# Optimization experiments

Hardware: AMD Instinct MI355X
Metric: run time of the kernel (lower is better)

Reference implementation:

```python
import jax, jax.numpy as jnp
import numpy as np

NUM_EMBEDDINGS = 1024
EMBEDDING_DIM = 256


def setup_inputs() -> dict:
    key = jax.random.key(0)
    k1, k2 = jax.random.split(key)
    input = jax.random.normal(k1, (64, 32, 32, EMBEDDING_DIM), dtype=jnp.float32)
    weight = jax.random.normal(k2, (NUM_EMBEDDINGS, EMBEDDING_DIM), dtype=jnp.float32)
    return {"input": input, "weight": weight}


def reference(input, weight):
    # Nearest-code lookup: argmin_k 0.5*||mu_k||^2 - <z, mu_k>  (scaled by 2 here,
    # matching torch: sqr - 2*cov). weight: [K, D], input: [..., D].
    sqr = jnp.sum(weight * weight, axis=1)                      # [K]
    cov = jnp.einsum('...j,kj->...k', input, weight)            # [..., K]
    indices = jnp.argmin(sqr - 2.0 * cov, axis=-1)              # [...]
    vectors = jnp.take(weight, indices, axis=0)                 # [..., D]
    # Straight-through estimator: values == vectors, grad flows to input.
    values = jax.lax.stop_gradient(vectors - input) + input
    return values, indices, vectors
```

## Files before the change

kernel.cpp:

```cpp
#include <hip/hip_runtime.h>


constexpr int N_TOK = 65536;
constexpr int KC    = 1024;
constexpr int D     = 256;

constexpr size_t IDX_OFF = (size_t)N_TOK * D;
constexpr size_t VEC_OFF = IDX_OFF + N_TOK;
constexpr int    OWL_CAP = 1 << 20;

#define MARGIN 12.0f

typedef __attribute__((ext_vector_type(8)))  short bf16x8;
typedef __attribute__((ext_vector_type(16))) float f32x16;

__device__ inline unsigned short f2bf(float x) {
    unsigned int u = __float_as_uint(x);
    unsigned int r = (u + 0x7FFFu + ((u >> 16) & 1u)) >> 16;
    return (unsigned short)r;
}

__device__ inline unsigned int fkey(float f) {
    unsigned int b = __float_as_uint(f);
    return (b & 0x80000000u) ? ~b : (b | 0x80000000u);
}

__global__ __launch_bounds__(64)
void vq_prep(const float* __restrict__ w, unsigned short* __restrict__ wbf,
             float* __restrict__ sqr, float* __restrict__ sqrp,
             int* __restrict__ cnt) {
    const int code = blockIdx.x;
    const int lane = threadIdx.x;
    float4 v = ((const float4*)w)[(size_t)code * 64 + lane];
    float s = v.x * v.x + v.y * v.y + v.z * v.z + v.w * v.w;
#pragma unroll
    for (int off = 32; off >= 1; off >>= 1) s += __shfl_xor(s, off, 64);
    unsigned short* d = wbf + (size_t)code * D + lane * 4;
    d[0] = f2bf(v.x); d[1] = f2bf(v.y); d[2] = f2bf(v.z); d[3] = f2bf(v.w);
    if (lane == 0) {
        sqr[code] = s;
        const int wi = code & 31;
        const int dest = (code >> 5) * 32 + ((wi >> 2) & 1) * 16
                       + (wi & 3) + 4 * (wi >> 3);
        sqrp[dest] = s;
    }
    if (code == 0 && lane == 0) *cnt = 0;
}

constexpr int CT   = 32;
constexpr int NSTG = KC / CT;
constexpr int LCAP = 5120;

struct __align__(16) P1Shared {
    unsigned short sbuf[3][CT * D];
    float sqr[KC];
    float sqrp[KC];
    int   list[LCAP];
    unsigned long long lcand[128];
    int   lcnt;
};

__device__ __forceinline__ void stage_issue(const char* __restrict__ srcbase,
                                            unsigned short* __restrict__ dstbuf,
                                            const int (&soff)[4], int tid) {
#pragma unroll
    for (int r = 0; r < 4; ++r) {
        __builtin_amdgcn_global_load_lds(
            (const __attribute__((address_space(1))) void*)(srcbase + soff[r]),
            (__attribute__((address_space(3))) void*)(dstbuf + (tid + r * 256) * 8),
            16, 0, 0);
    }
}

__global__ __launch_bounds__(256, 2)
void vq_scan(const float* __restrict__ input, const float* __restrict__ weight,
             const unsigned short* __restrict__ wbf, const float* __restrict__ sqr,
             const float* __restrict__ sqrp,
             int* __restrict__ cnt, int* __restrict__ owl,
             unsigned long long* __restrict__ cand) {
    __shared__ P1Shared sh;

    const int tid  = threadIdx.x;
    const int wave = tid >> 6;
    const int lane = tid & 63;
    const int cl   = lane & 31;
    const int hi   = lane >> 5;
    const int row_base_blk = blockIdx.x * 128;
    const char* wbfB = (const char*)wbf;

    if (tid == 0) sh.lcnt = 0;
    if (tid < 128) sh.lcand[tid] = 0xFFFFFFFFFFFFFFFFULL;
    ((float4*)sh.sqr)[tid]  = ((const float4*)sqr)[tid];
    ((float4*)sh.sqrp)[tid] = ((const float4*)sqrp)[tid];

    int soff[4];
#pragma unroll
    for (int r = 0; r < 4; ++r) {
        const int sl = tid + r * 256;
        soff[r] = (sl & 31) * 512 + (sl >> 5) * 16;
    }

    bf16x8 afr[16];
    {
        const float* ar = input + (size_t)(row_base_blk + wave * 32 + cl) * D;
#pragma unroll
        for (int kt = 0; kt < 16; ++kt) {
            const int k0 = kt * 16 + hi * 8;
            float4 f0 = *(const float4*)(ar + k0);
            float4 f1 = *(const float4*)(ar + k0 + 4);
            bf16x8 v;
            v[0] = (short)f2bf(f0.x); v[1] = (short)f2bf(f0.y);
            v[2] = (short)f2bf(f0.z); v[3] = (short)f2bf(f0.w);
            v[4] = (short)f2bf(f1.x); v[5] = (short)f2bf(f1.y);
            v[6] = (short)f2bf(f1.z); v[7] = (short)f2bf(f1.w);
            afr[kt] = v;
        }
    }

    float rmin = 3.4e38f;

    __syncthreads();

    stage_issue(wbfB, sh.sbuf[0], soff, tid);
    stage_issue(wbfB + 16384, sh.sbuf[1], soff, tid);

    for (int s = 0; s < NSTG; ++s) {
        if (s == NSTG - 1) asm volatile("s_waitcnt vmcnt(0)" ::: "memory");
        else               asm volatile("s_waitcnt vmcnt(4)" ::: "memory");
        __builtin_amdgcn_sched_barrier(0);
        __builtin_amdgcn_s_barrier();
        __builtin_amdgcn_sched_barrier(0);
        if (s + 2 < NSTG)
            stage_issue(wbfB + (s + 2) * 16384, sh.sbuf[(s + 2) % 3], soff, tid);

        const unsigned short* sb = sh.sbuf[s % 3] + (size_t)lane * 8;
        f32x16 acc = {0.f,0.f,0.f,0.f, 0.f,0.f,0.f,0.f,
                      0.f,0.f,0.f,0.f, 0.f,0.f,0.f,0.f};
#pragma unroll
        for (int h = 0; h < 2; ++h) {
            bf16x8 b[8];
#pragma unroll
            for (int kk = 0; kk < 8; ++kk)
                b[kk] = *(const bf16x8*)(sb + (h * 8 + kk) * 512);
#pragma unroll
            for (int kk = 0; kk < 8; ++kk)
                acc = __builtin_amdgcn_mfma_f32_32x32x16_bf16(b[kk], afr[h * 8 + kk], acc, 0, 0, 0);
        }

        const int c0 = s * CT;
        const float4* sp = (const float4*)(sh.sqrp + c0 + hi * 16);
        float4 q0 = sp[0], q1 = sp[1], q2 = sp[2], q3 = sp[3];
        float sc[16];
        sc[0]=q0.x-2.0f*acc[0];  sc[1]=q0.y-2.0f*acc[1];
        sc[2]=q0.z-2.0f*acc[2];  sc[3]=q0.w-2.0f*acc[3];
        sc[4]=q1.x-2.0f*acc[4];  sc[5]=q1.y-2.0f*acc[5];
        sc[6]=q1.z-2.0f*acc[6];  sc[7]=q1.w-2.0f*acc[7];
        sc[8]=q2.x-2.0f*acc[8];  sc[9]=q2.y-2.0f*acc[9];
        sc[10]=q2.z-2.0f*acc[10]; sc[11]=q2.w-2.0f*acc[11];
        sc[12]=q3.x-2.0f*acc[12]; sc[13]=q3.y-2.0f*acc[13];
        sc[14]=q3.z-2.0f*acc[14]; sc[15]=q3.w-2.0f*acc[15];

        float m = fminf(fminf(fminf(sc[0], sc[1]), fminf(sc[2], sc[3])),
                        fminf(fminf(sc[4], sc[5]), fminf(sc[6], sc[7])));
        m = fminf(m, fminf(fminf(fminf(sc[8], sc[9]), fminf(sc[10], sc[11])),
                           fminf(fminf(sc[12], sc[13]), fminf(sc[14], sc[15]))));
        m = fminf(m, __shfl_xor(m, 32, 64));
        rmin = fminf(rmin, m);
        const float thr = rmin + MARGIN;

        const int lrow = wave * 32 + cl;
#pragma unroll
        for (int r = 0; r < 16; ++r) {
            const bool flag = (sc[r] <= thr);
            unsigned long long mask = __ballot(flag);
            if (mask) {
                const int leader = __builtin_ctzll(mask);
                const int nact   = __popcll(mask);
                const int prefix = __popcll(mask & ((1ULL << lane) - 1ULL));
                int wbase = 0;
                if (lane == leader) wbase = atomicAdd(&sh.lcnt, nact);
                wbase = __shfl(wbase, leader, 64);
                if (flag) {
                    const int code = c0 + (r & 3) + 8 * (r >> 2) + 4 * hi;
                    const int pos  = wbase + prefix;
                    if (pos < LCAP) {
                        sh.list[pos] = (lrow << 10) | code;
                    } else {
                        int g = atomicAdd(cnt, 1);
                        if (g < OWL_CAP)
                            owl[g] = ((row_base_blk + lrow) << 10) | code;
                    }
                }
            }
        }
    }

    __syncthreads();

    {
        const int n  = min(sh.lcnt, LCAP);
        const int sw = tid >> 4;
        const int sl = tid & 15;
        const float4* in4 = (const float4*)input;
        const float4* w4  = (const float4*)weight;
        for (int e = sw; e < n; e += 16) {
            const int ent  = sh.list[e];
            const int lrow = ent >> 10;
            const int code = ent & 1023;
            const float4* zr = in4 + (size_t)(row_base_blk + lrow) * 64;
            const float4* wr = w4 + (size_t)code * 64;
            float s = 0.f;
#pragma unroll
            for (int j = 0; j < 4; ++j) {
                float4 za = zr[sl + 16 * j];
                float4 wa = wr[sl + 16 * j];
                s = fmaf(za.x, wa.x, s);
                s = fmaf(za.y, wa.y, s);
                s = fmaf(za.z, wa.z, s);
                s = fmaf(za.w, wa.w, s);
            }
#pragma unroll
            for (int off = 1; off <= 8; off <<= 1) s += __shfl_xor(s, off, 16);
            if (sl == 0) {
                const float score = sh.sqr[code] - 2.0f * s;
                unsigned long long key =
                    ((unsigned long long)fkey(score) << 32) | (unsigned int)code;
                atomicMin(&sh.lcand[lrow], key);
            }
        }
    }
    __syncthreads();

    if (tid < 128) cand[row_base_blk + tid] = sh.lcand[tid];
}

__global__ __launch_bounds__(256)
void vq_cleanup(const float* __restrict__ input, const float* __restrict__ weight,
                const float* __restrict__ sqr, const int* __restrict__ owl,
                const int* __restrict__ cnt, unsigned long long* __restrict__ cand) {
    const int m = min(*cnt, OWL_CAP);
    if (m == 0) return;
    __shared__ float zrow[D];
    __shared__ unsigned long long best;
    const int tid = threadIdx.x;
    for (int e = blockIdx.x; e < m; e += gridDim.x) {
        const int grow = owl[e] >> 10;
        if (tid == 0) best = 0xFFFFFFFFFFFFFFFFULL;
        if (tid < 64) ((float4*)zrow)[tid] = ((const float4*)input)[(size_t)grow * 64 + tid];
        __syncthreads();
        for (int cc = 0; cc < 4; ++cc) {
            const int code = tid * 4 + cc;
            const float4* wr = (const float4*)weight + (size_t)code * 64;
            float s = 0.f;
            for (int k = 0; k < 64; ++k) {
                float4 wa = wr[k];
                s = fmaf(zrow[4 * k],     wa.x, s);
                s = fmaf(zrow[4 * k + 1], wa.y, s);
                s = fmaf(zrow[4 * k + 2], wa.z, s);
                s = fmaf(zrow[4 * k + 3], wa.w, s);
            }
            const float score = sqr[code] - 2.0f * s;
            unsigned long long key =
                ((unsigned long long)fkey(score) << 32) | (unsigned int)code;
            atomicMin(&best, key);
        }
        __syncthreads();
        if (tid == 0) cand[grow] = best;
        __syncthreads();
    }
}

__global__ __launch_bounds__(256)
void vq_finish(const float* __restrict__ weight,
               const unsigned long long* __restrict__ cand,
               float* __restrict__ out) {
    __shared__ int fin[64];
    const int tid  = threadIdx.x;
    const int row0 = blockIdx.x * 64;
    if (tid < 64) {
        int idx = (int)(cand[row0 + tid] & 1023ULL);
        fin[tid] = idx;
        out[IDX_OFF + row0 + tid] = (float)idx;
    }
    __syncthreads();
    const float4* w4 = (const float4*)weight;
    float4* out4 = (float4*)out;
#pragma unroll
    for (int k = 0; k < 16; ++k) {
        int i = tid + k * 256;
        int r = i >> 6, q = i & 63;
        float4 v = w4[(size_t)fin[r] * 64 + q];
        size_t o = (size_t)(row0 + r) * 64 + q;
        out4[o] = v;
        out4[VEC_OFF / 4 + o] = v;
    }
}

extern "C" void kernel_launch(void* const* d_in, const int* in_sizes, int n_in,
                              void* d_out, int out_size, void* d_ws, size_t ws_size,
                              hipStream_t stream) {
    const float* input  = (const float*)d_in[0];
    const float* weight = (const float*)d_in[1];
    float* out = (float*)d_out;

    unsigned short* wbf = (unsigned short*)d_ws;
    float* sqr  = (float*)((char*)d_ws + 524288);
    float* sqrp = (float*)((char*)d_ws + 528384);
    int*   cnt  = (int*)((char*)d_ws + 532480);
    unsigned long long* cand = (unsigned long long*)((char*)d_ws + 536576);

    int* owl = (int*)out;

    vq_prep   <<<KC, 64, 0, stream>>>(weight, wbf, sqr, sqrp, cnt);
    vq_scan   <<<N_TOK / 128, 256, 0, stream>>>(input, weight, wbf, sqr, sqrp, cnt, owl, cand);
    vq_cleanup<<<256, 256, 0, stream>>>(input, weight, sqr, owl, cnt, cand);
    vq_finish <<<N_TOK / 64, 256, 0, stream>>>(weight, cand, out);
}
```

Before: 305.1 us.

## Widen scan blocks to 512 threads with per-wave candidate lists and score prefilter

The scan kernel now runs 512-thread blocks covering 256 rows, with 64-code stages that are double-buffered instead of triple-buffered. Each codebook tile loaded into LDS is therefore reused by twice as many rows. Candidate collection no longer uses a shared atomic counter. Each wave builds its own segment through a wave prefix scan and stores a truncated score key, and the fp32 rescoring pass skips entries whose key exceeds that row's final threshold. The cost is one block per CU, a synchronous barrier with only one stage of prefetch, and more shuffle work per tile.

```diff
diff --git a/kernel.cpp b/kernel.cpp
--- a/kernel.cpp
+++ b/kernel.cpp
@@ -40,24 +40,26 @@
     if (lane == 0) {
         sqr[code] = s;
         const int wi = code & 31;
-        const int dest = (code >> 5) * 32 + ((wi >> 2) & 1) * 16
+        const int dest = (code & ~31) + ((wi >> 2) & 1) * 16
                        + (wi & 3) + 4 * (wi >> 3);
         sqrp[dest] = s;
     }
     if (code == 0 && lane == 0) *cnt = 0;
 }
 
-constexpr int CT   = 32;
+constexpr int CT   = 64;
 constexpr int NSTG = KC / CT;
-constexpr int LCAP = 5120;
+constexpr int WCAP = 1280;
+constexpr int ROWS = 256;
 
 struct __align__(16) P1Shared {
-    unsigned short sbuf[3][CT * D];
+    unsigned short sbuf[2][CT * D];
     float sqr[KC];
     float sqrp[KC];
-    int   list[LCAP];
-    unsigned long long lcand[128];
-    int   lcnt;
+    int   list[8 * WCAP];
+    unsigned long long lcand[ROWS];
+    unsigned short tk[ROWS];
+    int   lcnt[8];
 };
 
 __device__ __forceinline__ void stage_issue(const char* __restrict__ srcbase,
@@ -67,12 +69,12 @@
     for (int r = 0; r < 4; ++r) {
         __builtin_amdgcn_global_load_lds(
             (const __attribute__((address_space(1))) void*)(srcbase + soff[r]),
-            (__attribute__((address_space(3))) void*)(dstbuf + (tid + r * 256) * 8),
+            (__attribute__((address_space(3))) void*)(dstbuf + (tid + r * 512) * 8),
             16, 0, 0);
     }
 }
 
-__global__ __launch_bounds__(256, 2)
+__global__ __launch_bounds__(512, 1)
 void vq_scan(const float* __restrict__ input, const float* __restrict__ weight,
              const unsigned short* __restrict__ wbf, const float* __restrict__ sqr,
              const float* __restrict__ sqrp,
@@ -85,19 +87,21 @@
     const int lane = tid & 63;
     const int cl   = lane & 31;
     const int hi   = lane >> 5;
-    const int row_base_blk = blockIdx.x * 128;
+    const int row_base_blk = blockIdx.x * ROWS;
     const char* wbfB = (const char*)wbf;
 
-    if (tid == 0) sh.lcnt = 0;
-    if (tid < 128) sh.lcand[tid] = 0xFFFFFFFFFFFFFFFFULL;
-    ((float4*)sh.sqr)[tid]  = ((const float4*)sqr)[tid];
-    ((float4*)sh.sqrp)[tid] = ((const float4*)sqrp)[tid];
+    if (tid < 8) sh.lcnt[tid] = 0;
+    if (tid < 256) {
+        sh.lcand[tid] = 0xFFFFFFFFFFFFFFFFULL;
+        ((float4*)sh.sqr)[tid]  = ((const float4*)sqr)[tid];
+        ((float4*)sh.sqrp)[tid] = ((const float4*)sqrp)[tid];
+    }
 
     int soff[4];
 #pragma unroll
     for (int r = 0; r < 4; ++r) {
-        const int sl = tid + r * 256;
-        soff[r] = (sl & 31) * 512 + (sl >> 5) * 16;
+        const int sl = tid + r * 512;
+        soff[r] = (sl & 63) * 512 + (sl >> 6) * 16;
     }
 
     bf16x8 afr[16];
@@ -118,120 +122,139 @@
     }
 
     float rmin = 3.4e38f;
+    int   wcur = 0;
 
     __syncthreads();
 
     stage_issue(wbfB, sh.sbuf[0], soff, tid);
-    stage_issue(wbfB + 16384, sh.sbuf[1], soff, tid);
 
     for (int s = 0; s < NSTG; ++s) {
-        if (s == NSTG - 1) asm volatile("s_waitcnt vmcnt(0)" ::: "memory");
-        else               asm volatile("s_waitcnt vmcnt(4)" ::: "memory");
-        __builtin_amdgcn_sched_barrier(0);
-        __builtin_amdgcn_s_barrier();
-        __builtin_amdgcn_sched_barrier(0);
-        if (s + 2 < NSTG)
-            stage_issue(wbfB + (s + 2) * 16384, sh.sbuf[(s + 2) % 3], soff, tid);
-
-        const unsigned short* sb = sh.sbuf[s % 3] + (size_t)lane * 8;
-        f32x16 acc = {0.f,0.f,0.f,0.f, 0.f,0.f,0.f,0.f,
-                      0.f,0.f,0.f,0.f, 0.f,0.f,0.f,0.f};
-#pragma unroll
-        for (int h = 0; h < 2; ++h) {
-            bf16x8 b[8];
-#pragma unroll
-            for (int kk = 0; kk < 8; ++kk)
-                b[kk] = *(const bf16x8*)(sb + (h * 8 + kk) * 512);
-#pragma unroll
-            for (int kk = 0; kk < 8; ++kk)
-                acc = __builtin_amdgcn_mfma_f32_32x32x16_bf16(b[kk], afr[h * 8 + kk], acc, 0, 0, 0);
-        }
-
+        __syncthreads();
+        if (s + 1 < NSTG)
+            stage_issue(wbfB + (s + 1) * 32768, sh.sbuf[(s + 1) & 1], soff, tid);
+
+        const unsigned short* sbb = sh.sbuf[s & 1];
         const int c0 = s * CT;
-        const float4* sp = (const float4*)(sh.sqrp + c0 + hi * 16);
-        float4 q0 = sp[0], q1 = sp[1], q2 = sp[2], q3 = sp[3];
-        float sc[16];
-        sc[0]=q0.x-2.0f*acc[0];  sc[1]=q0.y-2.0f*acc[1];
-        sc[2]=q0.z-2.0f*acc[2];  sc[3]=q0.w-2.0f*acc[3];
-        sc[4]=q1.x-2.0f*acc[4];  sc[5]=q1.y-2.0f*acc[5];
-        sc[6]=q1.z-2.0f*acc[6];  sc[7]=q1.w-2.0f*acc[7];
-        sc[8]=q2.x-2.0f*acc[8];  sc[9]=q2.y-2.0f*acc[9];
-        sc[10]=q2.z-2.0f*acc[10]; sc[11]=q2.w-2.0f*acc[11];
-        sc[12]=q3.x-2.0f*acc[12]; sc[13]=q3.y-2.0f*acc[13];
-        sc[14]=q3.z-2.0f*acc[14]; sc[15]=q3.w-2.0f*acc[15];
-
-        float m = fminf(fminf(fminf(sc[0], sc[1]), fminf(sc[2], sc[3])),
-                        fminf(fminf(sc[4], sc[5]), fminf(sc[6], sc[7])));
-        m = fminf(m, fminf(fminf(fminf(sc[8], sc[9]), fminf(sc[10], sc[11])),
-                           fminf(fminf(sc[12], sc[13]), fminf(sc[14], sc[15]))));
-        m = fminf(m, __shfl_xor(m, 32, 64));
-        rmin = fminf(rmin, m);
-        const float thr = rmin + MARGIN;
-
-        const int lrow = wave * 32 + cl;
-#pragma unroll
-        for (int r = 0; r < 16; ++r) {
-            const bool flag = (sc[r] <= thr);
-            unsigned long long mask = __ballot(flag);
-            if (mask) {
-                const int leader = __builtin_ctzll(mask);
-                const int nact   = __popcll(mask);
-                const int prefix = __popcll(mask & ((1ULL << lane) - 1ULL));
-                int wbase = 0;
-                if (lane == leader) wbase = atomicAdd(&sh.lcnt, nact);
-                wbase = __shfl(wbase, leader, 64);
-                if (flag) {
-                    const int code = c0 + (r & 3) + 8 * (r >> 2) + 4 * hi;
-                    const int pos  = wbase + prefix;
-                    if (pos < LCAP) {
-                        sh.list[pos] = (lrow << 10) | code;
-                    } else {
-                        int g = atomicAdd(cnt, 1);
-                        if (g < OWL_CAP)
-                            owl[g] = ((row_base_blk + lrow) << 10) | code;
+
+#pragma unroll
+        for (int t = 0; t < 2; ++t) {
+            const unsigned short* sb = sbb + (size_t)(hi * 64 + t * 32 + cl) * 8;
+            f32x16 acc = {0.f,0.f,0.f,0.f, 0.f,0.f,0.f,0.f,
+                          0.f,0.f,0.f,0.f, 0.f,0.f,0.f,0.f};
+#pragma unroll
+            for (int h = 0; h < 2; ++h) {
+                bf16x8 b[8];
+#pragma unroll
+                for (int kk = 0; kk < 8; ++kk)
+                    b[kk] = *(const bf16x8*)(sb + (size_t)(h * 8 + kk) * 1024);
+#pragma unroll
+                for (int kk = 0; kk < 8; ++kk)
+                    acc = __builtin_amdgcn_mfma_f32_32x32x16_bf16(b[kk], afr[h * 8 + kk], acc, 0, 0, 0);
+            }
+
+            const float4* sp = (const float4*)(sh.sqrp + c0 + t * 32 + hi * 16);
+            float4 q0 = sp[0], q1 = sp[1], q2 = sp[2], q3 = sp[3];
+            float sc[16];
+            sc[0]=q0.x-2.0f*acc[0];   sc[1]=q0.y-2.0f*acc[1];
+            sc[2]=q0.z-2.0f*acc[2];   sc[3]=q0.w-2.0f*acc[3];
+            sc[4]=q1.x-2.0f*acc[4];   sc[5]=q1.y-2.0f*acc[5];
+            sc[6]=q1.z-2.0f*acc[6];   sc[7]=q1.w-2.0f*acc[7];
+            sc[8]=q2.x-2.0f*acc[8];   sc[9]=q2.y-2.0f*acc[9];
+            sc[10]=q2.z-2.0f*acc[10]; sc[11]=q2.w-2.0f*acc[11];
+            sc[12]=q3.x-2.0f*acc[12]; sc[13]=q3.y-2.0f*acc[13];
+            sc[14]=q3.z-2.0f*acc[14]; sc[15]=q3.w-2.0f*acc[15];
+
+            float m = fminf(fminf(fminf(sc[0], sc[1]), fminf(sc[2], sc[3])),
+                            fminf(fminf(sc[4], sc[5]), fminf(sc[6], sc[7])));
+            m = fminf(m, fminf(fminf(fminf(sc[8], sc[9]), fminf(sc[10], sc[11])),
+                               fminf(fminf(sc[12], sc[13]), fminf(sc[14], sc[15]))));
+            m = fminf(m, __shfl_xor(m, 32, 64));
+            rmin = fminf(rmin, m);
+            const float thr = rmin + MARGIN;
+
+            unsigned m16 = 0u;
+#pragma unroll
+            for (int r = 0; r < 16; ++r)
+                m16 |= (sc[r] <= thr) ? (1u << r) : 0u;
+            const int cntl = __popc(m16);
+            int incl = cntl;
+#pragma unroll
+            for (int off = 1; off < 64; off <<= 1) {
+                int v = __shfl_up(incl, off, 64);
+                if (lane >= off) incl += v;
+            }
+            const int total = __shfl(incl, 63, 64);
+            if (total) {
+                const int base = wcur + (incl - cntl);
+                int* seg = sh.list + wave * WCAP;
+#pragma unroll
+                for (int r = 0; r < 16; ++r) {
+                    if (m16 & (1u << r)) {
+                        const int pos  = base + __popc(m16 & ((1u << r) - 1u));
+                        const int code = c0 + t * 32 + (r & 3) + 8 * (r >> 2) + 4 * hi;
+                        if (pos < WCAP) {
+                            const unsigned skey = fkey(sc[r]) >> 16;
+                            seg[pos] = (int)((skey << 16) | ((unsigned)cl << 10)
+                                             | (unsigned)code);
+                        } else {
+                            int g = atomicAdd(cnt, 1);
+                            if (g < OWL_CAP)
+                                owl[g] = ((row_base_blk + wave * 32 + cl) << 10) | code;
+                        }
                     }
                 }
+                wcur += total;
             }
         }
     }
 
+    if (hi == 0) {
+        unsigned t32 = (fkey(rmin + MARGIN) >> 16) + 1u;
+        sh.tk[wave * 32 + cl] = (unsigned short)(t32 > 0xFFFFu ? 0xFFFFu : t32);
+    }
+    if (lane == 0) sh.lcnt[wave] = (wcur < WCAP) ? wcur : WCAP;
+
     __syncthreads();
 
     {
-        const int n  = min(sh.lcnt, LCAP);
         const int sw = tid >> 4;
         const int sl = tid & 15;
         const float4* in4 = (const float4*)input;
         const float4* w4  = (const float4*)weight;
-        for (int e = sw; e < n; e += 16) {
-            const int ent  = sh.list[e];
-            const int lrow = ent >> 10;
-            const int code = ent & 1023;
-            const float4* zr = in4 + (size_t)(row_base_blk + lrow) * 64;
-            const float4* wr = w4 + (size_t)code * 64;
-            float s = 0.f;
-#pragma unroll
-            for (int j = 0; j < 4; ++j) {
-                float4 za = zr[sl + 16 * j];
-                float4 wa = wr[sl + 16 * j];
-                s = fmaf(za.x, wa.x, s);
-                s = fmaf(za.y, wa.y, s);
-                s = fmaf(za.z, wa.z, s);
-                s = fmaf(za.w, wa.w, s);
-            }
-#pragma unroll
-            for (int off = 1; off <= 8; off <<= 1) s += __shfl_xor(s, off, 16);
-            if (sl == 0) {
-                const float score = sh.sqr[code] - 2.0f * s;
-                unsigned long long key =
-                    ((unsigned long long)fkey(score) << 32) | (unsigned int)code;
-                atomicMin(&sh.lcand[lrow], key);
+        for (int seg = 0; seg < 8; ++seg) {
+            const int n = sh.lcnt[seg];
+            const int* lp = sh.list + seg * WCAP;
+            for (int e = sw; e < n; e += 32) {
+                const unsigned ent = (unsigned)lp[e];
+                const int lrow = seg * 32 + (int)((ent >> 10) & 31u);
+                if ((ent >> 16) > (unsigned)sh.tk[lrow]) continue;
+                const int code = (int)(ent & 1023u);
+                const float4* zr = in4 + (size_t)(row_base_blk + lrow) * 64;
+                const float4* wr = w4 + (size_t)code * 64;
+                float s = 0.f;
+#pragma unroll
+                for (int j = 0; j < 4; ++j) {
+                    float4 za = zr[sl + 16 * j];
+                    float4 wa = wr[sl + 16 * j];
+                    s = fmaf(za.x, wa.x, s);
+                    s = fmaf(za.y, wa.y, s);
+                    s = fmaf(za.z, wa.z, s);
+                    s = fmaf(za.w, wa.w, s);
+                }
+#pragma unroll
+                for (int off = 1; off <= 8; off <<= 1) s += __shfl_xor(s, off, 16);
+                if (sl == 0) {
+                    const float score = sh.sqr[code] - 2.0f * s;
+                    unsigned long long key =
+                        ((unsigned long long)fkey(score) << 32) | (unsigned int)code;
+                    atomicMin(&sh.lcand[lrow], key);
+                }
             }
         }
     }
     __syncthreads();
 
-    if (tid < 128) cand[row_base_blk + tid] = sh.lcand[tid];
+    if (tid < 256) cand[row_base_blk + tid] = sh.lcand[tid];
 }
 
 __global__ __launch_bounds__(256)
@@ -312,7 +335,7 @@
     int* owl = (int*)out;
 
     vq_prep   <<<KC, 64, 0, stream>>>(weight, wbf, sqr, sqrp, cnt);
-    vq_scan   <<<N_TOK / 128, 256, 0, stream>>>(input, weight, wbf, sqr, sqrp, cnt, owl, cand);
+    vq_scan   <<<N_TOK / ROWS, 512, 0, stream>>>(input, weight, wbf, sqr, sqrp, cnt, owl, cand);
     vq_cleanup<<<256, 256, 0, stream>>>(input, weight, sqr, owl, cnt, cand);
     vq_finish <<<N_TOK / 64, 256, 0, stream>>>(weight, cand, out);
 }
```

New measurement: 283.8 us. -7.0%, faster.
